# Kernel tuning notes

Measured on AMD Instinct MI355X. Metric: run time of the kernel, lower is better.

The kernel has to match this reference:

```python
import jax, jax.numpy as jnp
import numpy as np
import math

B, S, E, H = 2, 1024, 2560, 32
D = E // H  # 80


def setup_inputs() -> dict:
    key = jax.random.key(0)
    ks = jax.random.split(key, 10)
    hidden_states = jax.random.normal(ks[0], (B, S, E), dtype=jnp.float32)
    Wqkv = jax.random.normal(ks[1], (E, 3 * E), dtype=jnp.float32) * 0.02
    bqkv = jnp.zeros((3 * E,), dtype=jnp.float32)
    Wproj = jax.random.normal(ks[2], (E, E), dtype=jnp.float32) * 0.02
    bproj = jnp.zeros((E,), dtype=jnp.float32)
    # gate matrices: hadamard, pauli_x, pauli_z (all real branches in torch code)
    hadamard = jnp.array([[1.0, 1.0], [1.0, -1.0]], dtype=jnp.float32) / math.sqrt(2.0)
    pauli_x = jnp.array([[0.0, 1.0], [1.0, 0.0]], dtype=jnp.float32)
    pauli_z = jnp.array([[1.0, 0.0], [0.0, -1.0]], dtype=jnp.float32)
    gate_mats = jnp.stack([hadamard, pauli_x, pauli_z])  # (3,2,2)
    # phase_rotation init is zeros in torch; randomize slightly for nontrivial numerics
    gate_phases = jax.random.normal(ks[3], (3, D), dtype=jnp.float32) * 0.1
    gate_amps = jnp.ones((3, D), dtype=jnp.float32)
    quantum_phase = jax.random.normal(ks[4], (H,), dtype=jnp.float32) * 0.1
    interference_strength = jnp.float32(0.8)
    return {
        'hidden_states': hidden_states, 'Wqkv': Wqkv, 'bqkv': bqkv,
        'Wproj': Wproj, 'bproj': bproj, 'gate_mats': gate_mats,
        'gate_phases': gate_phases, 'gate_amps': gate_amps,
        'quantum_phase': quantum_phase,
        'interference_strength': interference_strength,
    }


def _gate_coeffs(gate_mats, gate_phases, gate_amps):
    # QuantumGate fwd: stack([x*cos(p), x*sin(p)], -1) @ G, summed over last axis, * amp
    # => per-dim scalar coeff: (cos(p)*(g00+g01) + sin(p)*(g10+g11)) * amp
    row0 = gate_mats[:, 0, 0] + gate_mats[:, 0, 1]  # (3,)
    row1 = gate_mats[:, 1, 0] + gate_mats[:, 1, 1]  # (3,)
    return (jnp.cos(gate_phases) * row0[:, None] + jnp.sin(gate_phases) * row1[:, None]) * gate_amps  # (3, D)


def reference(hidden_states, Wqkv, bqkv, Wproj, bproj, gate_mats, gate_phases, gate_amps, quantum_phase, interference_strength):
    scale = D ** -0.5
    qkv = hidden_states @ Wqkv + bqkv  # (B,S,3E)
    q, k, v = jnp.split(qkv, 3, axis=-1)
    # (B,H,S,D)
    q = q.reshape(B, S, H, D).transpose(0, 2, 1, 3)
    k = k.reshape(B, S, H, D).transpose(0, 2, 1, 3)
    v = v.reshape(B, S, H, D).transpose(0, 2, 1, 3)

    attn_scores = jnp.einsum('bhqd,bhkd->bhqk', q, k) * scale

    coeffs = _gate_coeffs(gate_mats, gate_phases, gate_amps)  # (3,D)
    # quantum attention per gate: (q * coeff_i) @ k^T * scale
    qa = jnp.einsum('gd,bhqd,bhkd->gbhqk', coeffs, q, k) * scale  # (3,B,H,S,S)
    interference = (qa[0] * qa[1] + qa[0] * qa[2] + qa[1] * qa[2]) * interference_strength
    attn_scores = attn_scores + interference / 3.0

    attn_probs = jax.nn.softmax(attn_scores, axis=-1)
    attn_probs = attn_probs * jnp.cos(quantum_phase)[None, :, None, None]

    attn_output = jnp.einsum('bhqk,bhkd->bhqd', attn_probs, v)
    attn_output = attn_output.transpose(0, 2, 1, 3).reshape(B, S, E)
    return attn_output @ Wproj + bproj
```

## Files before the change

### kernel.cpp

```cpp
#include <hip/hip_runtime.h>
#include <hip/hip_bf16.h>
#include <math.h>

#define S_  1024
#define E_  2560
#define H_  32
#define D_  80
#define E3_ 7680
#define M_  2048
#define QK_ 5120

typedef short bf16x8 __attribute__((ext_vector_type(8)));
typedef float f32x4  __attribute__((ext_vector_type(4)));

static __device__ __forceinline__ float bf2f(unsigned short u) {
    unsigned int i = ((unsigned int)u) << 16;
    float f; __builtin_memcpy(&f, &i, 4); return f;
}
static __device__ __forceinline__ unsigned short f2bf(float f) {
    unsigned int i; __builtin_memcpy(&i, &f, 4);
    i += 0x7fffu + ((i >> 16) & 1u);
    return (unsigned short)(i >> 16);
}

__global__ __launch_bounds__(256) void cvt_bf16_kernel(
    const float* __restrict__ in, unsigned short* __restrict__ out, int n8)
{
    int i = (blockIdx.x * 256 + threadIdx.x);
    if (i >= n8) return;
    const float* p = in + (size_t)i * 8;
    float4 a = *(const float4*)p;
    float4 b = *(const float4*)(p + 4);
    union { uint4 v; unsigned short s[8]; } o;
    o.s[0]=f2bf(a.x); o.s[1]=f2bf(a.y); o.s[2]=f2bf(a.z); o.s[3]=f2bf(a.w);
    o.s[4]=f2bf(b.x); o.s[5]=f2bf(b.y); o.s[6]=f2bf(b.z); o.s[7]=f2bf(b.w);
    *(uint4*)(out + (size_t)i * 8) = o.v;
}

__global__ __launch_bounds__(256) void transpose_bf16_kernel(
    const float* __restrict__ in, unsigned short* __restrict__ out, int R, int C)
{
    const int t = threadIdx.x;
    const int r0 = blockIdx.y * 64, c0 = blockIdx.x * 64;
    const int r4 = (t >> 4) * 4;
    const int c4 = (t & 15) * 4;
    float4 rows[4];
#pragma unroll
    for (int i = 0; i < 4; ++i)
        rows[i] = *(const float4*)&in[(size_t)(r0 + r4 + i) * C + c0 + c4];
    const float rv[4][4] = {
        {rows[0].x, rows[0].y, rows[0].z, rows[0].w},
        {rows[1].x, rows[1].y, rows[1].z, rows[1].w},
        {rows[2].x, rows[2].y, rows[2].z, rows[2].w},
        {rows[3].x, rows[3].y, rows[3].z, rows[3].w}};
#pragma unroll
    for (int j = 0; j < 4; ++j) {
        ushort4 o;
        o.x = f2bf(rv[0][j]); o.y = f2bf(rv[1][j]);
        o.z = f2bf(rv[2][j]); o.w = f2bf(rv[3][j]);
        *(ushort4*)&out[(size_t)(c0 + c4 + j) * R + r0 + r4] = o;
    }
}

template <bool A_F32, bool OUT_F32>
__global__ __launch_bounds__(256, 2) void mfma_gemm_kernel(
    const void* __restrict__ A, int lda,
    const unsigned short* __restrict__ Wt,
    const float* __restrict__ bias,
    void* __restrict__ dst0, int sd0,
    void* __restrict__ dst1, int sd1, int ncut,
    int K)
{
    __shared__ unsigned short As[128 * 40];
    __shared__ unsigned short Bs[128 * 40];

    const int t    = threadIdx.x;
    const int m0   = blockIdx.y * 128;
    const int n0   = blockIdx.x * 128;
    const int lane = t & 63, wave = t >> 6;
    const int quad = lane >> 4, l15 = lane & 15;
    const int mw   = (wave >> 1) * 64;
    const int nw   = (wave & 1) * 64;
    const int r    = t >> 1;
    const int hh   = (t & 1) * 16;

    f32x4 acc[4][4];
#pragma unroll
    for (int i = 0; i < 4; ++i)
#pragma unroll
        for (int j = 0; j < 4; ++j) acc[i][j] = (f32x4){0.f, 0.f, 0.f, 0.f};

    const size_t a_base = (size_t)(m0 + r) * lda + hh;
    const unsigned short* bp = Wt + (size_t)(n0 + r) * K + hh;

    for (int k0 = 0; k0 < K; k0 += 32) {
        uint4 a0, a1;
        if (A_F32) {
            const float* ap = (const float*)A + a_base + k0;
            float4 f0 = *(const float4*)ap;
            float4 f1 = *(const float4*)(ap + 4);
            float4 f2 = *(const float4*)(ap + 8);
            float4 f3 = *(const float4*)(ap + 12);
            union { uint4 v; unsigned short s[8]; } u0, u1;
            u0.s[0]=f2bf(f0.x); u0.s[1]=f2bf(f0.y); u0.s[2]=f2bf(f0.z); u0.s[3]=f2bf(f0.w);
            u0.s[4]=f2bf(f1.x); u0.s[5]=f2bf(f1.y); u0.s[6]=f2bf(f1.z); u0.s[7]=f2bf(f1.w);
            u1.s[0]=f2bf(f2.x); u1.s[1]=f2bf(f2.y); u1.s[2]=f2bf(f2.z); u1.s[3]=f2bf(f2.w);
            u1.s[4]=f2bf(f3.x); u1.s[5]=f2bf(f3.y); u1.s[6]=f2bf(f3.z); u1.s[7]=f2bf(f3.w);
            a0 = u0.v; a1 = u1.v;
        } else {
            const unsigned short* ap = (const unsigned short*)A + a_base + k0;
            a0 = *(const uint4*)ap;
            a1 = *(const uint4*)(ap + 8);
        }
        uint4 b0 = *(const uint4*)(bp + k0);
        uint4 b1 = *(const uint4*)(bp + k0 + 8);
        __syncthreads();
        *(uint4*)&As[r * 40 + hh]     = a0;
        *(uint4*)&As[r * 40 + hh + 8] = a1;
        *(uint4*)&Bs[r * 40 + hh]     = b0;
        *(uint4*)&Bs[r * 40 + hh + 8] = b1;
        __syncthreads();

        bf16x8 af[4], bfr[4];
#pragma unroll
        for (int i = 0; i < 4; ++i)
            af[i] = *(const bf16x8*)&As[(mw + i * 16 + l15) * 40 + quad * 8];
#pragma unroll
        for (int j = 0; j < 4; ++j)
            bfr[j] = *(const bf16x8*)&Bs[(nw + j * 16 + l15) * 40 + quad * 8];
#pragma unroll
        for (int i = 0; i < 4; ++i)
#pragma unroll
            for (int j = 0; j < 4; ++j)
                acc[i][j] = __builtin_amdgcn_mfma_f32_16x16x32_bf16(af[i], bfr[j], acc[i][j], 0, 0, 0);
    }

#pragma unroll
    for (int j = 0; j < 4; ++j) {
        const int col = n0 + nw + j * 16 + l15;
        const float bv = bias[col];
        if (OUT_F32) {
            float* dst = (float*)dst0;
#pragma unroll
            for (int i = 0; i < 4; ++i) {
                const int rowb = m0 + mw + i * 16 + quad * 4;
#pragma unroll
                for (int g = 0; g < 4; ++g)
                    dst[(size_t)(rowb + g) * sd0 + col] = acc[i][j][g] + bv;
            }
        } else {
            unsigned short* dst; int sd, cc;
            if (col < ncut) { dst = (unsigned short*)dst0; sd = sd0; cc = col; }
            else            { dst = (unsigned short*)dst1; sd = sd1; cc = col - ncut; }
#pragma unroll
            for (int i = 0; i < 4; ++i) {
                const int rowb = m0 + mw + i * 16 + quad * 4;
#pragma unroll
                for (int g = 0; g < 4; ++g)
                    dst[(size_t)(rowb + g) * sd + cc] = f2bf(acc[i][j][g] + bv);
            }
        }
    }
}

__global__ __launch_bounds__(256, 2) void attn_mfma_kernel(
    unsigned short* __restrict__ qk,
    const unsigned short* __restrict__ vsrc,
    const float* __restrict__ gmats,
    const float* __restrict__ gphases,
    const float* __restrict__ gamps,
    const float* __restrict__ qphase,
    const float* __restrict__ is_ptr)
{
    __shared__ unsigned short Ks[64 * 104];
    __shared__ unsigned short Vt[80 * 72];
    __shared__ unsigned short Ps[64 * 72];
    __shared__ float cs[240];

    const int t    = threadIdx.x;
    const int wave = t >> 6, lane = t & 63;
    const int quad = lane >> 4, l15 = lane & 15;
    const int qt = blockIdx.x & 15;
    const int bh = blockIdx.x >> 4;
    const int h  = bh & 31;
    const int b  = bh >> 5;

    const float scale = 0.111803398874989485f;
    const float c2    = scale * scale * is_ptr[0] * (1.0f / 3.0f);
    const float cosph = cosf(qphase[h]);

    if (t < 240) {
        int g = t / 80;
        float r0 = gmats[g*4+0] + gmats[g*4+1];
        float r1 = gmats[g*4+2] + gmats[g*4+3];
        cs[t] = (cosf(gphases[t]) * r0 + sinf(gphases[t]) * r1) * gamps[t];
    }

    const int srow = t >> 2;
    const int scg  = (t & 3) * 20;

    {
        const unsigned short* qp = qk + (size_t)(b * S_ + qt * 64 + srow) * QK_ + h * D_ + scg;
#pragma unroll
        for (int u = 0; u < 5; ++u)
            *(ushort4*)&Ks[srow * 104 + scg + 4 * u] = *(const ushort4*)(qp + 4 * u);
        *(ushort4*)&Ks[srow * 104 + 80 + (t & 3) * 4] = (ushort4){0, 0, 0, 0};
    }
    __syncthreads();

    bf16x8 afq[3], afg[3][3];
#pragma unroll
    for (int kc = 0; kc < 3; ++kc)
        afq[kc] = *(const bf16x8*)&Ks[(wave * 16 + l15) * 104 + quad * 8 + kc * 32];
#pragma unroll
    for (int g = 0; g < 3; ++g)
#pragma unroll
        for (int kc = 0; kc < 3; ++kc)
#pragma unroll
            for (int j = 0; j < 8; ++j) {
                int d = kc * 32 + quad * 8 + j;
                float c = (d < 80) ? cs[g * 80 + d] : 0.f;
                afg[g][kc][j] = (short)f2bf(bf2f((unsigned short)afq[kc][j]) * c);
            }

    f32x4 Ov[5];
#pragma unroll
    for (int nf = 0; nf < 5; ++nf) Ov[nf] = (f32x4){0.f, 0.f, 0.f, 0.f};
    float m_r[4] = {-INFINITY, -INFINITY, -INFINITY, -INFINITY};
    float l_r[4] = {0.f, 0.f, 0.f, 0.f};

    for (int kt = 0; kt < 16; ++kt) {
        __syncthreads();

        const unsigned short* kp = qk + (size_t)(b * S_ + kt * 64 + srow) * QK_ + E_ + h * D_ + scg;
#pragma unroll
        for (int u = 0; u < 5; ++u)
            *(ushort4*)&Ks[srow * 104 + scg + 4 * u] = *(const ushort4*)(kp + 4 * u);

        for (int s = t; s < 320; s += 256) {
            const int dg = s % 20, kg = s / 20;
            ushort4 rv[4];
#pragma unroll
            for (int i = 0; i < 4; ++i)
                rv[i] = *(const ushort4*)&vsrc[(size_t)(b * S_ + kt * 64 + kg * 4 + i) * E_ + h * D_ + dg * 4];
            const unsigned short rm[4][4] = {
                {rv[0].x, rv[0].y, rv[0].z, rv[0].w},
                {rv[1].x, rv[1].y, rv[1].z, rv[1].w},
                {rv[2].x, rv[2].y, rv[2].z, rv[2].w},
                {rv[3].x, rv[3].y, rv[3].z, rv[3].w}};
#pragma unroll
            for (int j = 0; j < 4; ++j) {
                ushort4 w = {rm[0][j], rm[1][j], rm[2][j], rm[3][j]};
                *(ushort4*)&Vt[(dg * 4 + j) * 72 + kg * 4] = w;
            }
        }
        __syncthreads();

        f32x4 sacc[4][4];
#pragma unroll
        for (int v = 0; v < 4; ++v)
#pragma unroll
            for (int nf = 0; nf < 4; ++nf) sacc[v][nf] = (f32x4){0.f, 0.f, 0.f, 0.f};
#pragma unroll
        for (int kc = 0; kc < 3; ++kc) {
            bf16x8 bk[4];
#pragma unroll
            for (int nf = 0; nf < 4; ++nf)
                bk[nf] = *(const bf16x8*)&Ks[(nf * 16 + l15) * 104 + quad * 8 + kc * 32];
#pragma unroll
            for (int nf = 0; nf < 4; ++nf)
                sacc[0][nf] = __builtin_amdgcn_mfma_f32_16x16x32_bf16(afq[kc], bk[nf], sacc[0][nf], 0, 0, 0);
#pragma unroll
            for (int g = 0; g < 3; ++g)
#pragma unroll
                for (int nf = 0; nf < 4; ++nf)
                    sacc[1+g][nf] = __builtin_amdgcn_mfma_f32_16x16x32_bf16(afg[g][kc], bk[nf], sacc[1+g][nf], 0, 0, 0);
        }

        float p[4][4];
        float mx[4] = {-INFINITY, -INFINITY, -INFINITY, -INFINITY};
#pragma unroll
        for (int nf = 0; nf < 4; ++nf)
#pragma unroll
            for (int r = 0; r < 4; ++r) {
                float s0 = sacc[1][nf][r], s1 = sacc[2][nf][r], s2 = sacc[3][nf][r];
                float s = sacc[0][nf][r] * scale + (s0 * s1 + s0 * s2 + s1 * s2) * c2;
                p[nf][r] = s;
                mx[r] = fmaxf(mx[r], s);
            }
#pragma unroll
        for (int r = 0; r < 4; ++r) {
            mx[r] = fmaxf(mx[r], __shfl_xor(mx[r], 1));
            mx[r] = fmaxf(mx[r], __shfl_xor(mx[r], 2));
            mx[r] = fmaxf(mx[r], __shfl_xor(mx[r], 4));
            mx[r] = fmaxf(mx[r], __shfl_xor(mx[r], 8));
        }
        float alpha[4];
#pragma unroll
        for (int r = 0; r < 4; ++r) {
            float m_new = fmaxf(m_r[r], mx[r]);
            alpha[r] = __expf(m_r[r] - m_new);
            m_r[r] = m_new;
        }
#pragma unroll
        for (int nf = 0; nf < 4; ++nf)
#pragma unroll
            for (int r = 0; r < 4; ++r)
                p[nf][r] = __expf(p[nf][r] - m_r[r]);
#pragma unroll
        for (int r = 0; r < 4; ++r) {
            float s = p[0][r] + p[1][r] + p[2][r] + p[3][r];
            s += __shfl_xor(s, 1);
            s += __shfl_xor(s, 2);
            s += __shfl_xor(s, 4);
            s += __shfl_xor(s, 8);
            l_r[r] = l_r[r] * alpha[r] + s;
        }

#pragma unroll
        for (int nf = 0; nf < 4; ++nf)
#pragma unroll
            for (int r = 0; r < 4; ++r)
                Ps[(wave * 16 + quad * 4 + r) * 72 + l15 + 16 * nf] = f2bf(p[nf][r]);
        __asm__ volatile("s_waitcnt lgkmcnt(0)" ::: "memory");

#pragma unroll
        for (int nf = 0; nf < 5; ++nf)
#pragma unroll
            for (int r = 0; r < 4; ++r) Ov[nf][r] *= alpha[r];

        bf16x8 ap[2];
#pragma unroll
        for (int kc = 0; kc < 2; ++kc)
            ap[kc] = *(const bf16x8*)&Ps[(wave * 16 + l15) * 72 + quad * 8 + kc * 32];
#pragma unroll
        for (int nf = 0; nf < 5; ++nf)
#pragma unroll
            for (int kc = 0; kc < 2; ++kc) {
                bf16x8 bv = *(const bf16x8*)&Vt[(nf * 16 + l15) * 72 + quad * 8 + kc * 32];
                Ov[nf] = __builtin_amdgcn_mfma_f32_16x16x32_bf16(ap[kc], bv, Ov[nf], 0, 0, 0);
            }
    }

    float inv[4];
#pragma unroll
    for (int r = 0; r < 4; ++r) inv[r] = cosph / l_r[r];
#pragma unroll
    for (int nf = 0; nf < 5; ++nf)
#pragma unroll
        for (int r = 0; r < 4; ++r)
            qk[(size_t)(b * S_ + qt * 64 + wave * 16 + quad * 4 + r) * QK_ + h * D_ + nf * 16 + l15]
                = f2bf(Ov[nf][r] * inv[r]);
}

extern "C" void kernel_launch(void* const* d_in, const int* in_sizes, int n_in,
                              void* d_out, int out_size, void* d_ws, size_t ws_size,
                              hipStream_t stream) {
    (void)in_sizes; (void)n_in; (void)out_size; (void)ws_size;
    const float* hidden  = (const float*)d_in[0];
    const float* Wqkv    = (const float*)d_in[1];
    const float* bqkv    = (const float*)d_in[2];
    const float* Wproj   = (const float*)d_in[3];
    const float* bproj   = (const float*)d_in[4];
    const float* gmats   = (const float*)d_in[5];
    const float* gphases = (const float*)d_in[6];
    const float* gamps   = (const float*)d_in[7];
    const float* qphase  = (const float*)d_in[8];
    const float* is_ptr  = (const float*)d_in[9];

    unsigned short* qk_ws  = (unsigned short*)d_ws;
    unsigned short* h_bf16 = (unsigned short*)((char*)d_ws + (size_t)M_ * QK_ * 2);
    unsigned short* Wt     = (unsigned short*)((char*)d_ws + (size_t)M_ * QK_ * 2 + (size_t)M_ * E_ * 2);
    unsigned short* v_buf  = (unsigned short*)d_out;

    dim3 blk(256);
    cvt_bf16_kernel<<<dim3((M_ * E_ / 8 + 255) / 256), blk, 0, stream>>>(hidden, h_bf16, M_ * E_ / 8);
    transpose_bf16_kernel<<<dim3(E3_/64, E_/64), blk, 0, stream>>>(Wqkv, Wt, E_, E3_);
    mfma_gemm_kernel<false, false><<<dim3(E3_/128, M_/128), blk, 0, stream>>>(
        h_bf16, E_, Wt, bqkv, qk_ws, QK_, v_buf, E_, QK_, E_);
    attn_mfma_kernel<<<dim3(2 * H_ * (S_/64)), blk, 0, stream>>>(
        qk_ws, v_buf, gmats, gphases, gamps, qphase, is_ptr);
    transpose_bf16_kernel<<<dim3(E_/64, E_/64), blk, 0, stream>>>(Wproj, Wt, E_, E_);
    mfma_gemm_kernel<false, true><<<dim3(E_/128, M_/128), blk, 0, stream>>>(
        qk_ws, QK_, Wt, bproj, d_out, E_, d_out, E_, E_, E_);
}
```

Before: 484.4 us.

## Prefetch next K/V tile into registers and remap workgroups across XCDs

```diff
diff --git a/kernel.cpp b/kernel.cpp
--- a/kernel.cpp
+++ b/kernel.cpp
@@ -75,8 +75,12 @@
     __shared__ unsigned short Bs[128 * 40];
 
     const int t    = threadIdx.x;
-    const int m0   = blockIdx.y * 128;
-    const int n0   = blockIdx.x * 128;
+    const int gx  = gridDim.x;
+    const int nwg = gx * gridDim.y;
+    int lin = blockIdx.y * gx + blockIdx.x;
+    lin = (lin & 7) * (nwg >> 3) + (lin >> 3);
+    const int m0   = (lin / gx) * 128;
+    const int n0   = (lin % gx) * 128;
     const int lane = t & 63, wave = t >> 6;
     const int quad = lane >> 4, l15 = lane & 15;
     const int mw   = (wave >> 1) * 64;
@@ -163,7 +167,7 @@
     }
 }
 
-__global__ __launch_bounds__(256, 2) void attn_mfma_kernel(
+__global__ __launch_bounds__(256, 4) void attn_mfma_kernel(
     unsigned short* __restrict__ qk,
     const unsigned short* __restrict__ vsrc,
     const float* __restrict__ gmats,
@@ -180,8 +184,10 @@
     const int t    = threadIdx.x;
     const int wave = t >> 6, lane = t & 63;
     const int quad = lane >> 4, l15 = lane & 15;
-    const int qt = blockIdx.x & 15;
-    const int bh = blockIdx.x >> 4;
+    const int lin0 = blockIdx.x;
+    const int lin  = ((lin0 & 7) << 7) | (lin0 >> 3);
+    const int qt = lin & 15;
+    const int bh = lin >> 4;
     const int h  = bh & 31;
     const int b  = bh >> 5;
 
@@ -199,6 +205,9 @@
     const int srow = t >> 2;
     const int scg  = (t & 3) * 20;
 
+    const int vkg  = t & 15;
+    const int vdg0 = t >> 4;
+
     {
         const unsigned short* qp = qk + (size_t)(b * S_ + qt * 64 + srow) * QK_ + h * D_ + scg;
 #pragma unroll
@@ -207,6 +216,23 @@
         *(ushort4*)&Ks[srow * 104 + 80 + (t & 3) * 4] = (ushort4){0, 0, 0, 0};
     }
     __syncthreads();
+
+    ushort4 kpre[5];
+    ushort4 vpre[8];
+    {
+        const unsigned short* kp = qk + (size_t)(b * S_ + srow) * QK_ + E_ + h * D_ + scg;
+#pragma unroll
+        for (int u = 0; u < 5; ++u) kpre[u] = *(const ushort4*)(kp + 4 * u);
+        const unsigned short* vb = vsrc + (size_t)(b * S_) * E_ + h * D_;
+#pragma unroll
+        for (int i = 0; i < 4; ++i)
+            vpre[i] = *(const ushort4*)(vb + (size_t)(vkg * 4 + i) * E_ + vdg0 * 4);
+        if (t < 64) {
+#pragma unroll
+            for (int i = 0; i < 4; ++i)
+                vpre[4 + i] = *(const ushort4*)(vb + (size_t)(vkg * 4 + i) * E_ + 64 + vdg0 * 4);
+        }
+    }
 
     bf16x8 afq[3], afg[3][3];
 #pragma unroll
@@ -232,29 +258,50 @@
     for (int kt = 0; kt < 16; ++kt) {
         __syncthreads();
 
-        const unsigned short* kp = qk + (size_t)(b * S_ + kt * 64 + srow) * QK_ + E_ + h * D_ + scg;
 #pragma unroll
         for (int u = 0; u < 5; ++u)
-            *(ushort4*)&Ks[srow * 104 + scg + 4 * u] = *(const ushort4*)(kp + 4 * u);
-
-        for (int s = t; s < 320; s += 256) {
-            const int dg = s % 20, kg = s / 20;
-            ushort4 rv[4];
-#pragma unroll
-            for (int i = 0; i < 4; ++i)
-                rv[i] = *(const ushort4*)&vsrc[(size_t)(b * S_ + kt * 64 + kg * 4 + i) * E_ + h * D_ + dg * 4];
+            *(ushort4*)&Ks[srow * 104 + scg + 4 * u] = kpre[u];
+
+        {
             const unsigned short rm[4][4] = {
-                {rv[0].x, rv[0].y, rv[0].z, rv[0].w},
-                {rv[1].x, rv[1].y, rv[1].z, rv[1].w},
-                {rv[2].x, rv[2].y, rv[2].z, rv[2].w},
-                {rv[3].x, rv[3].y, rv[3].z, rv[3].w}};
+                {vpre[0].x, vpre[0].y, vpre[0].z, vpre[0].w},
+                {vpre[1].x, vpre[1].y, vpre[1].z, vpre[1].w},
+                {vpre[2].x, vpre[2].y, vpre[2].z, vpre[2].w},
+                {vpre[3].x, vpre[3].y, vpre[3].z, vpre[3].w}};
 #pragma unroll
             for (int j = 0; j < 4; ++j) {
                 ushort4 w = {rm[0][j], rm[1][j], rm[2][j], rm[3][j]};
-                *(ushort4*)&Vt[(dg * 4 + j) * 72 + kg * 4] = w;
+                *(ushort4*)&Vt[(vdg0 * 4 + j) * 72 + vkg * 4] = w;
+            }
+        }
+        if (t < 64) {
+            const unsigned short rm[4][4] = {
+                {vpre[4].x, vpre[4].y, vpre[4].z, vpre[4].w},
+                {vpre[5].x, vpre[5].y, vpre[5].z, vpre[5].w},
+                {vpre[6].x, vpre[6].y, vpre[6].z, vpre[6].w},
+                {vpre[7].x, vpre[7].y, vpre[7].z, vpre[7].w}};
+#pragma unroll
+            for (int j = 0; j < 4; ++j) {
+                ushort4 w = {rm[0][j], rm[1][j], rm[2][j], rm[3][j]};
+                *(ushort4*)&Vt[(64 + vdg0 * 4 + j) * 72 + vkg * 4] = w;
             }
         }
         __syncthreads();
+
+        if (kt < 15) {
+            const unsigned short* kp = qk + (size_t)(b * S_ + (kt + 1) * 64 + srow) * QK_ + E_ + h * D_ + scg;
+#pragma unroll
+            for (int u = 0; u < 5; ++u) kpre[u] = *(const ushort4*)(kp + 4 * u);
+            const unsigned short* vb = vsrc + (size_t)(b * S_ + (kt + 1) * 64) * E_ + h * D_;
+#pragma unroll
+            for (int i = 0; i < 4; ++i)
+                vpre[i] = *(const ushort4*)(vb + (size_t)(vkg * 4 + i) * E_ + vdg0 * 4);
+            if (t < 64) {
+#pragma unroll
+                for (int i = 0; i < 4; ++i)
+                    vpre[4 + i] = *(const ushort4*)(vb + (size_t)(vkg * 4 + i) * E_ + 64 + vdg0 * 4);
+            }
+        }
 
         f32x4 sacc[4][4];
 #pragma unroll
```

Measured after the change: 728.2 us. 1.5x slower.
